# Kernel optimization log

Measured on AMD Instinct MI355X. Metric: run time of the kernel, lower is better.

The kernel has to match this reference:

```python
import jax, jax.numpy as jnp
import numpy as np

B = 4096          # batch_size
D_EMB = 16        # per-side embedding dim (embed_to_from width = 2*D_EMB)
D_HIGH = 784      # flattened high-dim feature size
NSR = 5           # negative_sample_rate
A = 1.576943      # UMAP _a
B_PARAM = 0.8950608  # UMAP _b
REPULSION = 1.0
EPS = 1e-4
GLOBAL_LOSS = 0.5
TOTAL_STEPS = 1000
BATCH_COUNT = 500  # fixed step for deterministic alpha/beta
WARMUP = int(0.05 * TOTAL_STEPS)


def _safe_sqrt(sq):
    # sqrt with zero (not NaN) gradient at 0, matching zero-distance pairs
    safe = jnp.where(sq > 0, sq, 1.0)
    return jnp.where(sq > 0, jnp.sqrt(safe), 0.0)


def _pairwise_dist(x):
    # ||x_i - x_j|| via gram trick; avoids materializing [N,N,D]
    sq = jnp.sum(x * x, axis=1)                      # [N]
    gram = x @ x.T                                   # [N,N]
    d2 = sq[:, None] + sq[None, :] - 2.0 * gram
    return _safe_sqrt(jnp.maximum(d2, 0.0))


def _umap_ce_loss(embed_to_from, perm):
    e_to, e_from = jnp.split(embed_to_from, 2, axis=1)   # [B, D_EMB] each
    neg_to = jnp.repeat(e_to, NSR, axis=0)               # [B*NSR, D_EMB]
    repeat_neg = jnp.repeat(e_from, NSR, axis=0)
    neg_from = repeat_neg[perm]                          # shuffled negatives
    d_pos = _safe_sqrt(jnp.sum((e_to - e_from) ** 2, axis=1))
    d_neg = _safe_sqrt(jnp.sum((neg_to - neg_from) ** 2, axis=1))
    dist = jnp.concatenate([d_pos, d_neg], axis=0)       # [B*(1+NSR)]
    p_dist = 1.0 / (1.0 + A * dist ** (2.0 * B_PARAM))
    p_graph = jnp.concatenate([jnp.ones(B, p_dist.dtype), jnp.zeros(B * NSR, p_dist.dtype)])
    attraction = -p_graph * jnp.log(jnp.clip(p_dist, EPS, 1.0))
    repellant = -(1.0 - p_graph) * jnp.log(jnp.clip(1.0 - p_dist, EPS, 1.0)) * REPULSION
    return jnp.mean(attraction + repellant)


def _global_feature_loss(embed_to_from, to_x):
    e_to = embed_to_from[:, :D_EMB]
    to_x = to_x.reshape(to_x.shape[0], -1)
    high_dis = _pairwise_dist(to_x)     # [N,N]
    low_dis = _pairwise_dist(e_to)      # [N,N]
    # row-wise pearson correlation between high_dis and low_dis
    h = high_dis - jnp.mean(high_dis, axis=1, keepdims=True)
    l = low_dis - jnp.mean(low_dis, axis=1, keepdims=True)
    num = jnp.sum(h * l, axis=1)
    den = jnp.sqrt(jnp.sum(h * h, axis=1)) * jnp.sqrt(jnp.sum(l * l, axis=1))
    corr = jnp.mean(num / den)
    return -corr


def _alpha_beta():
    if BATCH_COUNT >= WARMUP:
        if BATCH_COUNT <= 0.9 * TOTAL_STEPS:
            beta = max(0.0, GLOBAL_LOSS * (1 - BATCH_COUNT / (TOTAL_STEPS - WARMUP * 4)) ** 2)
        else:
            beta = 0.0
        alpha = max(0.0, 1 - beta)
    else:
        alpha = 0.0
        beta = GLOBAL_LOSS
    return alpha, beta


def setup_inputs() -> dict:
    key = jax.random.key(0)
    k1, k2, k3 = jax.random.split(key, 3)
    embed_to_from = jax.random.normal(k1, (B, 2 * D_EMB), dtype=jnp.float32)
    placeholder = jax.random.normal(k2, (B, D_HIGH), dtype=jnp.float32)
    perm = jax.random.permutation(k3, B * NSR).astype(jnp.int32)
    return {"embed_to_from": embed_to_from, "placeholder": placeholder, "perm": perm}


def reference(embed_to_from, placeholder, perm):
    loss = _umap_ce_loss(embed_to_from, perm)
    loss_g = _global_feature_loss(embed_to_from, placeholder)
    alpha, beta = _alpha_beta()
    return alpha * loss + beta * loss_g
```

## Files before the change

### kernel.cpp

```cpp
#include <hip/hip_runtime.h>
#include <hip/hip_bf16.h>
#include <math.h>

#define NB    4096
#define DH    784
#define KX8   832
#define NSR   5
#define NNEG  (NB*NSR)
#define NTOT  (NB + NNEG)

#define A_CONST 1.576943f
#define PEXP    1.7901216f
#define EPS_C   1.0e-4f
#define ALPHA_C 0.9296875f
#define BETA_C  0.0703125f

#define NBLK  528

typedef __hip_bfloat16 bf16;
typedef short bf16x8 __attribute__((ext_vector_type(8)));
typedef float f32x4  __attribute__((ext_vector_type(4)));
typedef float f32x2  __attribute__((ext_vector_type(2)));
typedef long long2v __attribute__((ext_vector_type(2)));

#define WS_XF8    0
#define WS_EBF    3407872
#define WS_SQX    3670016
#define WS_SQE    3686400
#define WS_ACC5   3702784
#define WS_UPART  8945664
#define WS_CNT    8946304

__device__ __forceinline__ void gl2lds16(const void* g, void* l) {
    __builtin_amdgcn_global_load_lds(
        (const __attribute__((address_space(1))) unsigned int*)g,
        (__attribute__((address_space(3))) unsigned int*)l,
        16, 0, 0);
}

__global__ void prep_fused(const float* __restrict__ X, const float* __restrict__ emb,
                           const int* __restrict__ perm, unsigned char* __restrict__ Xf8,
                           float* __restrict__ sqx, bf16* __restrict__ Ebf,
                           float* __restrict__ sqe, float* __restrict__ upart,
                           float* __restrict__ acc5, unsigned* __restrict__ cnt) {
    if (blockIdx.x == 0 && threadIdx.x == 0) *cnt = 0u;
    if (blockIdx.x < 1024) {
        const int wave = threadIdx.x >> 6, lane = threadIdx.x & 63;
        const int row = blockIdx.x * 4 + wave;
        const float4* xr = (const float4*)(X + (size_t)row * DH);
        int* xb = (int*)(Xf8 + (size_t)row * KX8);
        float s = 0.f;
        #pragma unroll
        for (int it = 0; it < 4; ++it) {
            const int idx = lane + it * 64;
            if (idx < 208) {
                const int c = idx >> 4, p = idx & 15;
                const int q = p >> 2, h = (p >> 1) & 1, w = p & 1;
                const int src = c * 16 + h * 8 + q * 2 + w;
                int pk = 0;
                if (src < 196) {
                    float4 v = xr[src];
                    s += v.x * v.x + v.y * v.y + v.z * v.z + v.w * v.w;
                    int lo = __builtin_amdgcn_cvt_pk_fp8_f32(v.x, v.y, 0, false);
                    pk = __builtin_amdgcn_cvt_pk_fp8_f32(v.z, v.w, lo, true);
                }
                xb[idx] = pk;
            }
        }
        #pragma unroll
        for (int off = 32; off; off >>= 1) s += __shfl_down(s, off, 64);
        if (lane == 0) sqx[row] = s;
        return;
    }
    const int ub = blockIdx.x - 1024;
    const int t = ub * 256 + threadIdx.x;
    if (t < 5 * NB) acc5[t] = 0.f;
    float val = 0.f;
    if (t < NB) {
        const float4* av = (const float4*)(emb + (size_t)t * 32);
        float4 t0 = av[0], t1 = av[1], t2 = av[2], t3 = av[3];
        float4 f0 = av[4], f1 = av[5], f2 = av[6], f3 = av[7];
        bf16* eb = Ebf + (size_t)t * 32;
        union { bf16 h[4]; ushort4 u; } cv;
        #define ST4(dst, q) cv.h[0]=__float2bfloat16(q.x); cv.h[1]=__float2bfloat16(q.y); \
                            cv.h[2]=__float2bfloat16(q.z); cv.h[3]=__float2bfloat16(q.w); \
                            *(ushort4*)(dst) = cv.u;
        ST4(eb,      t0) ST4(eb + 4,  t1) ST4(eb + 8,  t2) ST4(eb + 12, t3)
        #undef ST4
        ushort4 z = {0, 0, 0, 0};
        *(ushort4*)(eb + 16) = z; *(ushort4*)(eb + 20) = z;
        *(ushort4*)(eb + 24) = z; *(ushort4*)(eb + 28) = z;
        sqe[t] = t0.x*t0.x + t0.y*t0.y + t0.z*t0.z + t0.w*t0.w
               + t1.x*t1.x + t1.y*t1.y + t1.z*t1.z + t1.w*t1.w
               + t2.x*t2.x + t2.y*t2.y + t2.z*t2.z + t2.w*t2.w
               + t3.x*t3.x + t3.y*t3.y + t3.z*t3.z + t3.w*t3.w;
        float d2 = 0.f;
        #define D2(a, b) { float4 df = {a.x-b.x, a.y-b.y, a.z-b.z, a.w-b.w}; \
                           d2 += df.x*df.x + df.y*df.y + df.z*df.z + df.w*df.w; }
        D2(t0, f0) D2(t1, f1) D2(t2, f2) D2(t3, f3)
        #undef D2
        float d = sqrtf(d2);
        float p = 1.f / (1.f + A_CONST * powf(d, PEXP));
        val = -logf(fminf(fmaxf(p, EPS_C), 1.f));
    } else if (t < NTOT) {
        const int k = t - NB;
        const int ti = k / 5;
        const int fi = perm[k] / 5;
        const float4* at = (const float4*)(emb + (size_t)ti * 32);
        const float4* bt = (const float4*)(emb + (size_t)fi * 32 + 16);
        float d2 = 0.f;
        #pragma unroll
        for (int q = 0; q < 4; ++q) {
            float4 a = at[q], b = bt[q];
            float4 df = {a.x-b.x, a.y-b.y, a.z-b.z, a.w-b.w};
            d2 += df.x*df.x + df.y*df.y + df.z*df.z + df.w*df.w;
        }
        float d = sqrtf(d2);
        float p = 1.f / (1.f + A_CONST * powf(d, PEXP));
        val = -logf(fminf(fmaxf(1.f - p, EPS_C), 1.f));
    }
    #pragma unroll
    for (int off = 32; off; off >>= 1) val += __shfl_down(val, off, 64);
    __shared__ float ps[4];
    if ((threadIdx.x & 63) == 0) ps[threadIdx.x >> 6] = val;
    __syncthreads();
    if (threadIdx.x == 0) upart[ub] = ps[0] + ps[1] + ps[2] + ps[3];
}

__global__ __launch_bounds__(256, 2) void gram_kernel(
    const unsigned char* __restrict__ Xf8, const bf16* __restrict__ Ebf,
    const float* __restrict__ sqx, const float* __restrict__ sqe,
    float* __restrict__ acc5, const float* __restrict__ upart,
    unsigned* __restrict__ cnt, float* __restrict__ out) {
    __shared__ __align__(16) unsigned char smem[67584];
    float* sqxs = (float*)(smem + 65536);
    float* sqes = (float*)(smem + 66560);
    float* scr  = (float*)smem;

    int bi, bj;
    {
        const int k = blockIdx.x & 7;
        const int idx = blockIdx.x >> 3;
        int g = -1, r = 0;
        if (k < 6) {
            const int SG[6] = {0,0,0,1,1,2}, SH[6] = {1,2,3,2,3,3};
            if (idx < 64) { bi = SG[k]*8 + (idx>>3); bj = SH[k]*8 + (idx&7); }
            else {
                const int DG[6] = {1,0,3,1,3,3};
                const int DR[6] = {32,34,30,34,32,34};
                g = DG[k]; r = DR[k] + (idx - 64);
            }
        } else if (k == 6) {
            if (idx < 34) { g = 0; r = idx; } else { g = 1; r = idx - 34; }
        } else {
            if (idx < 36) { g = 2; r = idx; } else { g = 3; r = idx - 36; }
        }
        if (g >= 0) {
            int a = 0;
            while (r >= 8 - a) { r -= 8 - a; ++a; }
            bi = g * 8 + a; bj = g * 8 + a + r;
        }
    }
    const int i0 = bi * 128, j0 = bj * 128;

    const int tid  = threadIdx.x;
    const int wave = tid >> 6;
    const int lane = tid & 63;
    const int wy = wave >> 1, wx = wave & 1;
    const int quad = lane >> 4, l15 = lane & 15;

    f32x4 acc[4][4];
    #pragma unroll
    for (int a = 0; a < 4; ++a)
        #pragma unroll
        for (int b = 0; b < 4; ++b)
            acc[a][b] = (f32x4){0.f, 0.f, 0.f, 0.f};

    if (tid < 128) {
        sqxs[tid] = sqx[i0 + tid];
        sqes[tid] = sqe[i0 + tid];
    }
    __syncthreads();

    const int gsb = (((lane & 3) ^ ((lane >> 3) & 3))) * 16;
    const unsigned char* gAw = Xf8 + (size_t)(i0 + wy * 64 + (lane >> 2)) * KX8 + gsb;
    const unsigned char* gBw = Xf8 + (size_t)(j0 + wx * 64 + (lane >> 2)) * KX8 + gsb;
    unsigned char* wbuf = smem + wave * 16384;

#define STAGE_X(b, t) { \
        const unsigned char* ga = gAw + (size_t)(t) * 64; \
        const unsigned char* gb = gBw + (size_t)(t) * 64; \
        unsigned char* la = wbuf + (b) * 8192; \
        unsigned char* lb = la + 4096; \
        gl2lds16(ga,              la);        gl2lds16(ga + 16 * KX8,  la + 1024); \
        gl2lds16(ga + 32 * KX8,   la + 2048); gl2lds16(ga + 48 * KX8,  la + 3072); \
        gl2lds16(gb,              lb);        gl2lds16(gb + 16 * KX8,  lb + 1024); \
        gl2lds16(gb + 32 * KX8,   lb + 2048); gl2lds16(gb + 48 * KX8,  lb + 3072); }

    STAGE_X(0, 0)
    STAGE_X(1, 1)

    const int key = (l15 >> 1) & 3;
    const int boX = ((quad ^ key) << 4);

    #pragma unroll
    for (int t = 0; t < 13; ++t) {
        if (t < 12) { asm volatile("s_waitcnt vmcnt(8)" ::: "memory"); }
        else        { asm volatile("s_waitcnt vmcnt(0)" ::: "memory"); }
        const unsigned char* la = wbuf + (t & 1) * 8192;
        long2v aF[4], bF[4];
        #pragma unroll
        for (int mi = 0; mi < 4; ++mi)
            aF[mi] = *(const long2v*)(la + (mi * 16 + l15) * 64 + boX);
        #pragma unroll
        for (int ni = 0; ni < 4; ++ni)
            bF[ni] = *(const long2v*)(la + 4096 + (ni * 16 + l15) * 64 + boX);
        asm volatile("s_waitcnt lgkmcnt(0)" ::: "memory");
        __builtin_amdgcn_sched_barrier(0);
        if (t < 11) STAGE_X(t & 1, t + 2)
        #pragma unroll
        for (int mi = 0; mi < 4; ++mi)
            #pragma unroll
            for (int ni = 0; ni < 4; ++ni) {
                acc[mi][ni] = __builtin_amdgcn_mfma_f32_16x16x32_fp8_fp8(
                    aF[mi][0], bF[ni][0], acc[mi][ni], 0, 0, 0);
                acc[mi][ni] = __builtin_amdgcn_mfma_f32_16x16x32_fp8_fp8(
                    aF[mi][1], bF[ni][1], acc[mi][ni], 0, 0, 0);
            }
    }
#undef STAGE_X

    const unsigned char* Eb = (const unsigned char*)Ebf;
    bf16x8 afE[4], bfrE[4];
    #pragma unroll
    for (int mi = 0; mi < 4; ++mi)
        afE[mi] = *(const bf16x8*)(Eb + (size_t)(i0 + wy * 64 + mi * 16 + l15) * 64 + quad * 16);
    #pragma unroll
    for (int ni = 0; ni < 4; ++ni)
        bfrE[ni] = *(const bf16x8*)(Eb + (size_t)(j0 + wx * 64 + ni * 16 + l15) * 64 + quad * 16);
    float sqxj[4], sqej[4];
    #pragma unroll
    for (int ni = 0; ni < 4; ++ni) {
        const int jl = wx * 64 + ni * 16 + l15;
        sqxj[ni] = sqxs[jl]; sqej[ni] = sqes[jl];
    }
    __syncthreads();

    float cst[4][5];
    #pragma unroll
    for (int ni = 0; ni < 4; ++ni)
        #pragma unroll
        for (int c = 0; c < 5; ++c) cst[ni][c] = 0.f;

    #pragma unroll
    for (int mi = 0; mi < 4; ++mi) {
        f32x4 aE[4];
        #pragma unroll
        for (int ni = 0; ni < 4; ++ni) {
            f32x4 z = (f32x4){0.f, 0.f, 0.f, 0.f};
            aE[ni] = __builtin_amdgcn_mfma_f32_16x16x32_bf16(afE[mi], bfrE[ni], z, 0, 0, 0);
        }
        const int ilb = wy * 64 + mi * 16 + quad * 4;
        float sqxi[4], sqei[4];
        #pragma unroll
        for (int r = 0; r < 4; ++r) { sqxi[r] = sqxs[ilb + r]; sqei[r] = sqes[ilb + r]; }
        float rs[5][4];
        #pragma unroll
        for (int c = 0; c < 5; ++c)
            #pragma unroll
            for (int r = 0; r < 4; ++r) rs[c][r] = 0.f;
        #pragma unroll
        for (int ni = 0; ni < 4; ++ni) {
            const int j = j0 + wx * 64 + ni * 16 + l15;
            #pragma unroll
            for (int r = 0; r < 4; ++r) {
                const int i = i0 + ilb + r;
                float H, L;
                if (i == j) { H = 0.f; L = 0.f; }
                else {
                    float d2  = sqxi[r] + sqxj[ni] - 2.0f * acc[mi][ni][r];
                    H = sqrtf(fmaxf(d2, 0.f));
                    float d2e = sqei[r] + sqej[ni] - 2.0f * aE[ni][r];
                    L = sqrtf(fmaxf(d2e, 0.f));
                }
                rs[0][r] += H; rs[1][r] += H * H; rs[2][r] += L;
                rs[3][r] += L * L; rs[4][r] += H * L;
                cst[ni][0] += H; cst[ni][1] += H * H; cst[ni][2] += L;
                cst[ni][3] += L * L; cst[ni][4] += H * L;
            }
        }
        #pragma unroll
        for (int c = 0; c < 5; ++c)
            #pragma unroll
            for (int r = 0; r < 4; ++r)
                scr[(size_t)((((wx * 5 + c) << 5) + (wy << 4) + (quad << 2) + r)) * 18 + l15]
                    = rs[c][r];
        __syncthreads();
        for (int o = tid; o < 160; o += 256) {
            const int c = o >> 5, li = o & 31;
            const float* p0 = scr + (size_t)((c << 5) + li) * 18;
            const float* p1 = scr + (size_t)(((5 + c) << 5) + li) * 18;
            float s = 0.f;
            #pragma unroll
            for (int k = 0; k < 16; k += 2) {
                f32x2 v0 = *(const f32x2*)&p0[k]; s += v0.x + v0.y;
                f32x2 v1 = *(const f32x2*)&p1[k]; s += v1.x + v1.y;
            }
            const int iloc = ((li >> 4) << 6) + mi * 16 + (li & 15);
            unsafeAtomicAdd(&acc5[(size_t)c * NB + (i0 + iloc)], s);
        }
        __syncthreads();
    }

    if (bi != bj) {
        #pragma unroll
        for (int ni = 0; ni < 4; ++ni) {
            const int jl = wx * 64 + ni * 16 + l15;
            #pragma unroll
            for (int c = 0; c < 5; ++c)
                scr[(size_t)(c * 128 + jl) * 9 + (wy << 2) + quad] = cst[ni][c];
        }
        __syncthreads();
        for (int o = tid; o < 640; o += 256) {
            const int c = o >> 7, j = o & 127;
            const float* p = scr + (size_t)(c * 128 + j) * 9;
            float s = ((p[0] + p[1]) + (p[2] + p[3])) + ((p[4] + p[5]) + (p[6] + p[7]));
            unsafeAtomicAdd(&acc5[(size_t)c * NB + (j0 + j)], s);
        }
    }

    __shared__ int lastFlag;
    __syncthreads();
    if (tid == 0) {
        __threadfence();
        lastFlag = (atomicAdd(cnt, 1u) == (unsigned)(NBLK - 1));
    }
    __syncthreads();
    if (lastFlag) {
        __threadfence();
        const float invN = 1.0f / (float)NB;
        float v = 0.f;
        #pragma unroll
        for (int rr = 0; rr < 16; ++rr) {
            const int r = tid + rr * 256;
            const float a  = acc5[0 * NB + r];
            const float b  = acc5[1 * NB + r];
            const float c2 = acc5[2 * NB + r];
            const float d  = acc5[3 * NB + r];
            const float e  = acc5[4 * NB + r];
            float num = e - a * c2 * invN;
            float vh  = fmaxf(b - a * a * invN, 0.f);
            float vl  = fmaxf(d - c2 * c2 * invN, 0.f);
            v += num / (sqrtf(vh) * sqrtf(vl));
        }
        v *= (-BETA_C * invN);
        if (tid < 96) v += upart[tid] * (ALPHA_C / (float)NTOT);
        #pragma unroll
        for (int off = 32; off; off >>= 1) v += __shfl_down(v, off, 64);
        float* fin = (float*)smem;
        __syncthreads();
        if ((tid & 63) == 0) fin[tid >> 6] = v;
        __syncthreads();
        if (tid == 0)
            out[0] = (fin[0] + fin[1]) + (fin[2] + fin[3]);
    }
}

extern "C" void kernel_launch(void* const* d_in, const int* in_sizes, int n_in,
                              void* d_out, int out_size, void* d_ws, size_t ws_size,
                              hipStream_t stream) {
    const float* emb  = (const float*)d_in[0];
    const float* ph   = (const float*)d_in[1];
    const int*   perm = (const int*)d_in[2];
    float* out = (float*)d_out;

    char* ws = (char*)d_ws;
    unsigned char* Xf8 = (unsigned char*)(ws + WS_XF8);
    bf16*  Ebf    = (bf16*) (ws + WS_EBF);
    float* sqx    = (float*)(ws + WS_SQX);
    float* sqe    = (float*)(ws + WS_SQE);
    float* acc5   = (float*)(ws + WS_ACC5);
    float* upart  = (float*)(ws + WS_UPART);
    unsigned* cnt = (unsigned*)(ws + WS_CNT);

    prep_fused<<<1120, 256, 0, stream>>>(ph, emb, perm, Xf8, sqx, Ebf, sqe, upart, acc5, cnt);
    gram_kernel<<<NBLK, 256, 0, stream>>>(Xf8, Ebf, sqx, sqe, acc5, upart, cnt, out);
}
```

Measured before the change: 116.6 us.

## Share block-wide triple-buffered LDS tiles in gram kernel and raise occupancy

```diff
diff --git a/kernel.cpp b/kernel.cpp
--- a/kernel.cpp
+++ b/kernel.cpp
@@ -16,6 +16,7 @@
 #define BETA_C  0.0703125f
 
 #define NBLK  528
+#define BUFB  16384
 
 typedef __hip_bfloat16 bf16;
 typedef short bf16x8 __attribute__((ext_vector_type(8)));
@@ -127,14 +128,16 @@
     if (threadIdx.x == 0) upart[ub] = ps[0] + ps[1] + ps[2] + ps[3];
 }
 
-__global__ __launch_bounds__(256, 2) void gram_kernel(
+__global__ __launch_bounds__(256, 3) void gram_kernel(
     const unsigned char* __restrict__ Xf8, const bf16* __restrict__ Ebf,
     const float* __restrict__ sqx, const float* __restrict__ sqe,
     float* __restrict__ acc5, const float* __restrict__ upart,
     unsigned* __restrict__ cnt, float* __restrict__ out) {
-    __shared__ __align__(16) unsigned char smem[67584];
-    float* sqxs = (float*)(smem + 65536);
-    float* sqes = (float*)(smem + 66560);
+    __shared__ __align__(16) unsigned char smem[51200];
+    unsigned char* As = smem;
+    unsigned char* Bs = smem + 3 * 8192;
+    float* sqxs = (float*)(smem + 49152);
+    float* sqes = (float*)(smem + 50176);
     float* scr  = (float*)smem;
 
     int bi, bj;
@@ -176,48 +179,46 @@
         for (int b = 0; b < 4; ++b)
             acc[a][b] = (f32x4){0.f, 0.f, 0.f, 0.f};
 
+    const int rA  = lane >> 2;
+    const int gsb = (((lane & 3) ^ ((lane >> 3) & 3))) * 16;
+    const unsigned char* gA0 = Xf8 + (size_t)(i0 + wave * 32 + rA) * KX8 + gsb;
+    const unsigned char* gA1 = Xf8 + (size_t)(i0 + wave * 32 + 16 + rA) * KX8 + gsb;
+    const unsigned char* gB0 = Xf8 + (size_t)(j0 + wave * 32 + rA) * KX8 + gsb;
+    const unsigned char* gB1 = Xf8 + (size_t)(j0 + wave * 32 + 16 + rA) * KX8 + gsb;
+
     if (tid < 128) {
-        sqxs[tid] = sqx[i0 + tid];
-        sqes[tid] = sqe[i0 + tid];
-    }
-    __syncthreads();
-
-    const int gsb = (((lane & 3) ^ ((lane >> 3) & 3))) * 16;
-    const unsigned char* gAw = Xf8 + (size_t)(i0 + wy * 64 + (lane >> 2)) * KX8 + gsb;
-    const unsigned char* gBw = Xf8 + (size_t)(j0 + wx * 64 + (lane >> 2)) * KX8 + gsb;
-    unsigned char* wbuf = smem + wave * 16384;
-
-#define STAGE_X(b, t) { \
-        const unsigned char* ga = gAw + (size_t)(t) * 64; \
-        const unsigned char* gb = gBw + (size_t)(t) * 64; \
-        unsigned char* la = wbuf + (b) * 8192; \
-        unsigned char* lb = la + 4096; \
-        gl2lds16(ga,              la);        gl2lds16(ga + 16 * KX8,  la + 1024); \
-        gl2lds16(ga + 32 * KX8,   la + 2048); gl2lds16(ga + 48 * KX8,  la + 3072); \
-        gl2lds16(gb,              lb);        gl2lds16(gb + 16 * KX8,  lb + 1024); \
-        gl2lds16(gb + 32 * KX8,   lb + 2048); gl2lds16(gb + 48 * KX8,  lb + 3072); }
-
-    STAGE_X(0, 0)
-    STAGE_X(1, 1)
+        sqxs[tid] = sqx[i0 + tid]; sqxs[128 + tid] = sqx[j0 + tid];
+        sqes[tid] = sqe[i0 + tid]; sqes[128 + tid] = sqe[j0 + tid];
+    }
+    __syncthreads();
+
+#define STAGE_X(buf) { \
+        unsigned char* la = As + (buf) * 8192 + wave * 2048; \
+        unsigned char* lb = Bs + (buf) * 8192 + wave * 2048; \
+        gl2lds16(gA0, la); gl2lds16(gA1, la + 1024); \
+        gl2lds16(gB0, lb); gl2lds16(gB1, lb + 1024); \
+        gA0 += 64; gA1 += 64; gB0 += 64; gB1 += 64; }
+
+    STAGE_X(0)
+    STAGE_X(1)
 
     const int key = (l15 >> 1) & 3;
     const int boX = ((quad ^ key) << 4);
 
     #pragma unroll
     for (int t = 0; t < 13; ++t) {
-        if (t < 12) { asm volatile("s_waitcnt vmcnt(8)" ::: "memory"); }
+        if (t < 12) { asm volatile("s_waitcnt vmcnt(4)" ::: "memory"); }
         else        { asm volatile("s_waitcnt vmcnt(0)" ::: "memory"); }
-        const unsigned char* la = wbuf + (t & 1) * 8192;
+        __builtin_amdgcn_s_barrier();
+        const int cur = (t % 3) * 8192;
+        if (t < 11) { const int nb = ((t + 2) % 3); STAGE_X(nb) }
         long2v aF[4], bF[4];
         #pragma unroll
         for (int mi = 0; mi < 4; ++mi)
-            aF[mi] = *(const long2v*)(la + (mi * 16 + l15) * 64 + boX);
+            aF[mi] = *(const long2v*)&As[cur + (wy * 64 + mi * 16 + l15) * 64 + boX];
         #pragma unroll
         for (int ni = 0; ni < 4; ++ni)
-            bF[ni] = *(const long2v*)(la + 4096 + (ni * 16 + l15) * 64 + boX);
-        asm volatile("s_waitcnt lgkmcnt(0)" ::: "memory");
-        __builtin_amdgcn_sched_barrier(0);
-        if (t < 11) STAGE_X(t & 1, t + 2)
+            bF[ni] = *(const long2v*)&Bs[cur + (wx * 64 + ni * 16 + l15) * 64 + boX];
         #pragma unroll
         for (int mi = 0; mi < 4; ++mi)
             #pragma unroll
@@ -242,7 +243,7 @@
     #pragma unroll
     for (int ni = 0; ni < 4; ++ni) {
         const int jl = wx * 64 + ni * 16 + l15;
-        sqxj[ni] = sqxs[jl]; sqej[ni] = sqes[jl];
+        sqxj[ni] = sqxs[128 + jl]; sqej[ni] = sqes[128 + jl];
     }
     __syncthreads();
 
```

New measurement: 119.3 us. +2.4%, slower.
